# Kernel optimization log

Hardware: AMD Instinct MI355X
Metric: run time of the kernel (lower is better)

The kernel has to match this reference:

```python
import jax, jax.numpy as jnp
import numpy as np
from jax.scipy.special import logsumexp

S, L = 32768, 512  # seq_len, label_num


def setup_inputs() -> dict:
    key = jax.random.key(0)
    k1, k2, k3 = jax.random.split(key, 3)
    logit = jax.random.normal(k1, (S, L), dtype=jnp.float32)   # emissions [S, L]
    labels = jax.random.randint(k2, (S,), 0, L)                # gold path [S]
    T = jax.random.normal(k3, (L, L), dtype=jnp.float32)       # T[next, prev]
    return {"logit": logit, "labels": labels, "T": T}


def _crf_loss(logit, T, labels):
    # Forward algorithm: alpha_t[j] = logsumexp_i(alpha_{t-1}[i] + T[j, i]) + feat_t[j]
    alpha0 = logit[0]

    def step(alpha, feat):
        new_alpha = logsumexp(alpha[None, :] + T, axis=1) + feat  # [L]
        return new_alpha, None

    alpha_final, _ = jax.lax.scan(step, alpha0, logit[1:])
    log_Z = logsumexp(alpha_final)

    # Gold path score: feat_0[y0] + sum_{t>0} (feat_t[y_t] + T[y_t, y_{t-1}])
    emit = logit[0, labels[0]] + jnp.sum(logit[jnp.arange(1, logit.shape[0]), labels[1:]])
    trans = jnp.sum(T[labels[1:], labels[:-1]])
    gold = emit + trans
    return log_Z - gold


def reference(logit, labels, T):
    return _crf_loss(logit, T, labels)
```

## Files before the change

### kernel.cpp

```cpp
#include <hip/hip_runtime.h>
#include <stdint.h>


#define S_LEN 32768
#define L 512
#define CH 8
#define NCF 4096
#define NB  256
#define TPB 1024
#define LN448 6.104793232f
#define LN2   0.6931471806f

#define OFF_EAF  0
#define OFF_EAB  (256*1024)
#define OFF_G    (512*1024)
#define OFF_H    (OFF_G + NCF*512*2)
#define OFF_LSE  (OFF_H + NCF*512*2)
#define OFF_GOLD (OFF_LSE + (2*NCF+8)*4)

#define PL_A   0
#define PL_B   8192
#define SPA    16384
#define SPB    17664
#define LF     19456
#define SMEM_TOTAL (19456 + 4*32768)

typedef float v4f __attribute__((ext_vector_type(4)));

__device__ __forceinline__ float b2f(unsigned short u){
  return __uint_as_float(((unsigned)u) << 16);
}
__device__ __forceinline__ unsigned short f2b(float x){
  unsigned u = __float_as_uint(x);
  return (unsigned short)((u + 0x7fffu + ((u >> 16) & 1u)) >> 16);
}
__device__ __forceinline__ unsigned char to_fp8(float v){
  int u = __builtin_amdgcn_cvt_pk_fp8_f32(v, v, 0, false);
  return (unsigned char)(u & 0xff);
}

__device__ __forceinline__ void gl2lds16(const void* g, void* l){
  __builtin_amdgcn_global_load_lds(
      (const __attribute__((address_space(1))) void*)g,
      (__attribute__((address_space(3))) void*)l, 16, 0, 0);
}

__device__ __forceinline__ void lds_sync(){
  asm volatile("s_waitcnt lgkmcnt(0)" ::: "memory");
  __builtin_amdgcn_sched_barrier(0);
  __builtin_amdgcn_s_barrier();
  __builtin_amdgcn_sched_barrier(0);
}
__device__ __forceinline__ void sync2(){
  asm volatile("s_waitcnt vmcnt(2) lgkmcnt(0)" ::: "memory");
  __builtin_amdgcn_sched_barrier(0);
  __builtin_amdgcn_s_barrier();
  __builtin_amdgcn_sched_barrier(0);
}
__device__ __forceinline__ void sync0(){
  asm volatile("s_waitcnt vmcnt(0) lgkmcnt(0)" ::: "memory");
  __builtin_amdgcn_sched_barrier(0);
  __builtin_amdgcn_s_barrier();
  __builtin_amdgcn_sched_barrier(0);
}

__device__ __forceinline__ float waveMax(float v){
  #pragma unroll
  for (int off = 32; off >= 1; off >>= 1) v = fmaxf(v, __shfl_xor(v, off));
  return v;
}
__device__ __forceinline__ float waveSum(float v){
  #pragma unroll
  for (int off = 32; off >= 1; off >>= 1) v += __shfl_xor(v, off);
  return v;
}

__device__ __forceinline__ float blockSum16(float v, float* sred){
  #pragma unroll
  for (int off = 32; off >= 1; off >>= 1) v += __shfl_xor(v, off);
  int wid = threadIdx.x >> 6, lane = threadIdx.x & 63;
  if (lane == 0) sred[wid] = v;
  __syncthreads();
  if (threadIdx.x < 16) {
    float t = sred[threadIdx.x];
    t += __shfl_xor(t, 8); t += __shfl_xor(t, 4);
    t += __shfl_xor(t, 2); t += __shfl_xor(t, 1);
    if (threadIdx.x == 0) sred[16] = t;
  }
  __syncthreads();
  float r = sred[16];
  __syncthreads();
  return r;
}
__device__ __forceinline__ float blockSum8(float v, float* sred){
  #pragma unroll
  for (int off = 32; off >= 1; off >>= 1) v += __shfl_xor(v, off);
  int wid = threadIdx.x >> 6, lane = threadIdx.x & 63;
  if (lane == 0) sred[wid] = v;
  __syncthreads();
  if (threadIdx.x < 8) {
    float t = sred[threadIdx.x];
    t += __shfl_xor(t, 4); t += __shfl_xor(t, 2); t += __shfl_xor(t, 1);
    if (threadIdx.x == 0) sred[8] = t;
  }
  __syncthreads();
  float r = sred[8];
  __syncthreads();
  return r;
}

extern "C" __global__ __launch_bounds__(TPB)
void crf_prep(const float* __restrict__ logit,
              const int* __restrict__ labels,
              const float* __restrict__ T,
              unsigned char* __restrict__ EAf,
              unsigned char* __restrict__ EAb,
              float* __restrict__ part){
  __shared__ float sredG[17];
  const int tidx = threadIdx.x;
  {
    int tid = blockIdx.x*TPB + tidx;
    int r    = tid & 7;
    int lane = (tid >> 3) & 63;
    int kt   = (tid >> 9) & 15;
    int R16  = tid >> 13;
    int j = R16*16 + (lane & 15);
    int i = kt*32 + ((lane >> 4) << 3) + r;
    EAf[tid] = to_fp8(2.0f * __expf(T[j*L + i]));
    EAb[tid] = to_fp8(2.0f * __expf(T[i*L + j]));
  }
  {
    float acc = 0.f;
    if (tidx < 128) {
      int t = blockIdx.x*128 + tidx;
      int yt = labels[t];
      float v = logit[(size_t)t*L + yt];
      if (t > 0) v += T[yt*L + labels[t-1]];
      acc = v;
    }
    float s = blockSum16(acc, sredG);
    if (tidx == 0) part[blockIdx.x] = s;
  }
}

extern "C" __global__ __launch_bounds__(TPB, 4)
void crf_chunks(const float* __restrict__ logit,
                const unsigned char* __restrict__ EAf,
                const unsigned char* __restrict__ EAb,
                unsigned short* __restrict__ G,
                unsigned short* __restrict__ H){
  extern __shared__ __align__(16) char smem[];

  const int tidx = threadIdx.x;
  const int w    = tidx >> 6;
  const int lane = tidx & 63;
  const int quad = lane >> 4;
  const int cl   = lane & 15;
  const bool fwd = (blockIdx.x < NB/2);
  const int  b   = fwd ? blockIdx.x : (blockIdx.x - NB/2);
  const int  base = (fwd ? 0 : 1) + b*32;
  const int  cgA  = base + cl;
  const int  cgB  = cgA + 16;
  const int  cgcA = min(cgA, NCF-1);
  const int  cgcB = min(cgB, NCF-1);
  const bool isc0 = fwd && (cgA == 0);
  const int  jrow0 = w*32 + quad*4;

  const int  cgsA = min(base + w,      NCF-1);
  const int  cgsB = min(base + 16 + w, NCF-1);
  const unsigned so = ((unsigned)(lane*16)) ^ ((unsigned)((w & 7) << 4));

  const long* EAp = (const long*)(fwd ? EAf : EAb);
  long eA[2][16];
  #pragma unroll
  for (int mt = 0; mt < 2; ++mt)
    #pragma unroll
    for (int kt = 0; kt < 16; ++kt)
      eA[mt][kt] = EAp[(((w*2 + mt)*16) + kt)*64 + lane];

  const int pladdr = (jrow0 >> 5)*512 + ((((jrow0 >> 3) & 3)*16 + cl) << 3)
                   + (jrow0 & 7);
  const int bbb = lane*8;
  const int scl = (cl & 7) << 4;
  const int ib  = w*128 + quad*16;
  const int fa0 = LF + cl*2048 + (ib ^ scl);
  const int fa1 = LF + cl*2048 + ((ib + 64) ^ scl);

  auto stage = [&](int tile, int ks){
    int cgs = tile ? cgsB : cgsA;
    int t = fwd ? (cgs*CH + ks) : (cgs*CH + CH - 2 - ks);
    const char* row = (const char*)logit + (size_t)t*(L*4);
    char* dst = smem + (LF + ((ks & 1) << 16) + (tile << 15) + w*2048);
    gl2lds16(row + so, dst);
    gl2lds16(row + 1024 + so, dst + 1024);
  };
  auto wmax = [&](v4f x0, v4f x1, int spoff){
    float mx = fmaxf(fmaxf(fmaxf(x0[0],x0[1]),fmaxf(x0[2],x0[3])),
                     fmaxf(fmaxf(x1[0],x1[1]),fmaxf(x1[2],x1[3])));
    mx = fmaxf(mx, __shfl_xor(mx, 16));
    mx = fmaxf(mx, __shfl_xor(mx, 32));
    if (quad == 0) *(float*)(smem + spoff + cl*80 + w*4) = mx;
  };
  auto s2 = [&](v4f x0, v4f x1, int spoff, int ploff, float& m){
    const char* spb = smem + spoff + cl*80;
    float4 q0 = *(const float4*)spb;
    float4 q1 = *(const float4*)(spb + 16);
    float4 q2 = *(const float4*)(spb + 32);
    float4 q3 = *(const float4*)(spb + 48);
    float M = fmaxf(fmaxf(fmaxf(fmaxf(q0.x,q0.y),fmaxf(q0.z,q0.w)),
                          fmaxf(fmaxf(q1.x,q1.y),fmaxf(q1.z,q1.w))),
                    fmaxf(fmaxf(fmaxf(q2.x,q2.y),fmaxf(q2.z,q2.w)),
                          fmaxf(fmaxf(q3.x,q3.y),fmaxf(q3.z,q3.w))));
    float sc = 448.0f / M;
    int u0 = __builtin_amdgcn_cvt_pk_fp8_f32(x0[0]*sc, x0[1]*sc, 0, false);
    u0     = __builtin_amdgcn_cvt_pk_fp8_f32(x0[2]*sc, x0[3]*sc, u0, true);
    *(int*)(smem + ploff + pladdr) = u0;
    int u1 = __builtin_amdgcn_cvt_pk_fp8_f32(x1[0]*sc, x1[1]*sc, 0, false);
    u1     = __builtin_amdgcn_cvt_pk_fp8_f32(x1[2]*sc, x1[3]*sc, u1, true);
    *(int*)(smem + ploff + pladdr + 256) = u1;
    m += __logf(M) - LN448;
  };
  auto fmul = [&](v4f& x0, v4f& x1, int fbase, bool anchor){
    const char* fb = smem + fbase;
    float4 q0 = *(const float4*)(fb + fa0);
    float4 q1 = *(const float4*)(fb + fa1);
    float f0=__expf(q0.x), f1=__expf(q0.y), f2=__expf(q0.z), f3=__expf(q0.w);
    float g0=__expf(q1.x), g1=__expf(q1.y), g2=__expf(q1.z), g3=__expf(q1.w);
    if (anchor) {
      x0 = (v4f){f0,f1,f2,f3};  x1 = (v4f){g0,g1,g2,g3};
    } else {
      x0 = (v4f){x0[0]*f0, x0[1]*f1, x0[2]*f2, x0[3]*f3};
      x1 = (v4f){x1[0]*g0, x1[1]*g1, x1[2]*g2, x1[3]*g3};
    }
  };
  auto store_out = [&](v4f x0, v4f x1, float m, int cg, bool anchor){
    if (cg <= NCF-1) {
      float madj = m - (anchor ? (float)(CH-1) : (float)CH)*LN2;
      unsigned short* dst = (fwd ? G : H) + (size_t)cg*L + jrow0;
      unsigned long long pv =
           (unsigned long long)f2b(__logf(x0[0]) + madj)
        | ((unsigned long long)f2b(__logf(x0[1]) + madj) << 16)
        | ((unsigned long long)f2b(__logf(x0[2]) + madj) << 32)
        | ((unsigned long long)f2b(__logf(x0[3]) + madj) << 48);
      *(unsigned long long*)dst = pv;
      pv = (unsigned long long)f2b(__logf(x1[0]) + madj)
        | ((unsigned long long)f2b(__logf(x1[1]) + madj) << 16)
        | ((unsigned long long)f2b(__logf(x1[2]) + madj) << 32)
        | ((unsigned long long)f2b(__logf(x1[3]) + madj) << 48);
      *(unsigned long long*)(dst + 16) = pv;
    }
  };

  stage(0, 0);  stage(1, 0);

  v4f vA0, vA1, vB0, vB1;
  if (fwd) {
    vA0 = (v4f){1.f,1.f,1.f,1.f}; vA1 = vA0; vB0 = vA0; vB1 = vA0;
  } else {
    const float* ip = logit + (size_t)(cgcA*CH + CH - 1)*L + jrow0;
    float4 x0 = *(const float4*)ip, x1 = *(const float4*)(ip + 16);
    vA0 = (v4f){__expf(x0.x),__expf(x0.y),__expf(x0.z),__expf(x0.w)};
    vA1 = (v4f){__expf(x1.x),__expf(x1.y),__expf(x1.z),__expf(x1.w)};
    ip = logit + (size_t)(cgcB*CH + CH - 1)*L + jrow0;
    x0 = *(const float4*)ip; x1 = *(const float4*)(ip + 16);
    vB0 = (v4f){__expf(x0.x),__expf(x0.y),__expf(x0.z),__expf(x0.w)};
    vB1 = (v4f){__expf(x1.x),__expf(x1.y),__expf(x1.z),__expf(x1.w)};
  }
  float mA = 0.0f, mB = 0.0f;

  wmax(vA0, vA1, SPA);
  wmax(vB0, vB1, SPB);
  lds_sync();
  s2(vA0, vA1, SPA, PL_A, mA);
  sync2();

  #pragma unroll
  for (int k = 0; k < CH; ++k) {
    const bool last = (k == CH-1);
    {
      if (fwd ? (k+1 <= CH-1) : (k+1 <= CH-2)) stage(0, k+1);
      v4f a0 = (v4f){0.f,0.f,0.f,0.f};
      v4f a1 = (v4f){0.f,0.f,0.f,0.f};
      #pragma unroll
      for (int kt = 0; kt < 16; ++kt) {
        long bbv = *(const long*)(smem + PL_A + bbb + kt*512);
        a0 = __builtin_amdgcn_mfma_f32_16x16x32_fp8_fp8(eA[0][kt], bbv, a0, 0, 0, 0);
        a1 = __builtin_amdgcn_mfma_f32_16x16x32_fp8_fp8(eA[1][kt], bbv, a1, 0, 0, 0);
      }
      s2(vB0, vB1, SPB, PL_B, mB);
      if (fwd || !last) fmul(a0, a1, ((k & 1) << 16), k == 0 && isc0);
      if (k == 0 && isc0) mA = 0.0f;
      if (last) {
        store_out(a0, a1, mA, cgA, isc0);
      } else {
        vA0 = a0; vA1 = a1;
        wmax(vA0, vA1, SPA);
      }
      if (k >= CH-2) sync0(); else sync2();
    }
    {
      if (fwd ? (k+1 <= CH-1) : (k+1 <= CH-2)) stage(1, k+1);
      v4f b0 = (v4f){0.f,0.f,0.f,0.f};
      v4f b1 = (v4f){0.f,0.f,0.f,0.f};
      #pragma unroll
      for (int kt = 0; kt < 16; ++kt) {
        long bbv = *(const long*)(smem + PL_B + bbb + kt*512);
        b0 = __builtin_amdgcn_mfma_f32_16x16x32_fp8_fp8(eA[0][kt], bbv, b0, 0, 0, 0);
        b1 = __builtin_amdgcn_mfma_f32_16x16x32_fp8_fp8(eA[1][kt], bbv, b1, 0, 0, 0);
      }
      if (!last) s2(vA0, vA1, SPA, PL_A, mA);
      if (fwd || !last) fmul(b0, b1, ((k & 1) << 16) + 32768, false);
      if (last) {
        store_out(b0, b1, mB, cgB, false);
      } else {
        vB0 = b0; vB1 = b1;
        wmax(vB0, vB1, SPB);
        sync2();
      }
    }
  }
}

extern "C" __global__ __launch_bounds__(512)
void crf_lse(const unsigned short* __restrict__ G,
             const unsigned short* __restrict__ H,
             float* __restrict__ lsebuf){
  const int tidx = threadIdx.x;
  const int w    = tidx >> 6;
  const int lane = tidx & 63;
  const int g    = blockIdx.x*8 + w;
  const int j8   = lane*8;
  if (g == 0) {
    const unsigned short* p = G + (size_t)(NCF-1)*L + j8;
    ushort4 a = *(const ushort4*)p, bq = *(const ushort4*)(p + 4);
    float v[8] = { b2f(a.x),b2f(a.y),b2f(a.z),b2f(a.w),
                   b2f(bq.x),b2f(bq.y),b2f(bq.z),b2f(bq.w) };
    float mx = v[0];
    #pragma unroll
    for (int r = 1; r < 8; ++r) mx = fmaxf(mx, v[r]);
    mx = waveMax(mx);
    float s = 0.f;
    #pragma unroll
    for (int r = 0; r < 8; ++r) s += __expf(v[r] - mx);
    s = waveSum(s);
    if (lane == 0) lsebuf[2*NCF] = mx + __logf(s);
  } else {
    const unsigned short* hp = H + (size_t)g*L + j8;
    const unsigned short* gp = G + (size_t)(g-1)*L + j8;
    ushort4 ha = *(const ushort4*)hp, hb = *(const ushort4*)(hp + 4);
    ushort4 ga = *(const ushort4*)gp, gb = *(const ushort4*)(gp + 4);
    float hv[8] = { b2f(ha.x),b2f(ha.y),b2f(ha.z),b2f(ha.w),
                    b2f(hb.x),b2f(hb.y),b2f(hb.z),b2f(hb.w) };
    float gv[8] = { b2f(ga.x),b2f(ga.y),b2f(ga.z),b2f(ga.w),
                    b2f(gb.x),b2f(gb.y),b2f(gb.z),b2f(gb.w) };
    float m1 = -3.0e38f, m2 = -3.0e38f;
    #pragma unroll
    for (int r = 0; r < 8; ++r) {
      float a = hv[r] + gv[r];
      m1 = fmaxf(m1, a); m2 = fmaxf(m2, hv[r]);
    }
    m1 = waveMax(m1); m2 = waveMax(m2);
    float s1 = 0.f, s2 = 0.f;
    #pragma unroll
    for (int r = 0; r < 8; ++r) {
      s1 += __expf(hv[r] + gv[r] - m1);
      s2 += __expf(hv[r] - m2);
    }
    s1 = waveSum(s1); s2 = waveSum(s2);
    if (lane == 0) {
      lsebuf[g]       = m1 + __logf(s1);
      lsebuf[NCF + g] = m2 + __logf(s2);
    }
  }
}

extern "C" __global__ __launch_bounds__(512)
void crf_final(const float* __restrict__ lsebuf,
               const float* __restrict__ part,
               float* __restrict__ out){
  __shared__ float sredG[9];
  const int tidx = threadIdx.x;
  float acc = 0.f;
  for (int c = tidx; c < NCF; c += 512)
    if (c >= 1) acc += lsebuf[c] - lsebuf[NCF + c];
  if (tidx < NB) acc -= part[tidx];
  float s = blockSum8(acc, sredG);
  if (tidx == 0) out[0] = lsebuf[2*NCF] + s;
}

extern "C" void kernel_launch(void* const* d_in, const int* in_sizes, int n_in,
                              void* d_out, int out_size, void* d_ws, size_t ws_size,
                              hipStream_t stream){
  const float* logit = (const float*)d_in[0];
  const int* labels  = (const int*)d_in[1];
  const float* T     = (const float*)d_in[2];
  float* out = (float*)d_out;
  char* ws = (char*)d_ws;
  unsigned char* EAf = (unsigned char*)(ws + OFF_EAF);
  unsigned char* EAb = (unsigned char*)(ws + OFF_EAB);
  unsigned short* G  = (unsigned short*)(ws + OFF_G);
  unsigned short* H  = (unsigned short*)(ws + OFF_H);
  float* lsebuf = (float*)(ws + OFF_LSE);
  float* part   = (float*)(ws + OFF_GOLD);

  static bool attr_set = false;
  if (!attr_set) {
    (void)hipFuncSetAttribute((const void*)crf_chunks,
                        hipFuncAttributeMaxDynamicSharedMemorySize, SMEM_TOTAL);
    attr_set = true;
  }

  crf_prep  <<<NB, TPB, 0, stream>>>(logit, labels, T, EAf, EAb, part);
  crf_chunks<<<NB, TPB, SMEM_TOTAL, stream>>>(logit, EAf, EAb, G, H);
  crf_lse   <<<NCF/8, 512, 0, stream>>>(G, H, lsebuf);
  crf_final <<<1, 512, 0, stream>>>(lsebuf, part, out);
}
```

Before: 136.9 us.

## Merge ping-pong chain halves into one joint MFMA step per iteration

Replaces the staggered A/B ping-pong schedule, where one chain's MFMAs overlapped the other chain's reduction and normalisation, with a single step per iteration that runs both chains' MFMAs interleaved. Both chains then do their max-reduction and scaling together, so each iteration has two barriers instead of the earlier staggered sync2/sync0 pattern. The loop is no longer force-unrolled and every wait now drains all outstanding global loads (vmcnt(0)). This gives the scheduler more independent MFMA chains to interleave, but it removes the overlap between matrix work and the reduction phases and waits fully on staged loads each step.

```diff
diff --git a/kernel.cpp b/kernel.cpp
--- a/kernel.cpp
+++ b/kernel.cpp
@@ -47,12 +47,6 @@
 
 __device__ __forceinline__ void lds_sync(){
   asm volatile("s_waitcnt lgkmcnt(0)" ::: "memory");
-  __builtin_amdgcn_sched_barrier(0);
-  __builtin_amdgcn_s_barrier();
-  __builtin_amdgcn_sched_barrier(0);
-}
-__device__ __forceinline__ void sync2(){
-  asm volatile("s_waitcnt vmcnt(2) lgkmcnt(0)" ::: "memory");
   __builtin_amdgcn_sched_barrier(0);
   __builtin_amdgcn_s_barrier();
   __builtin_amdgcn_sched_barrier(0);
@@ -272,51 +266,44 @@
   wmax(vB0, vB1, SPB);
   lds_sync();
   s2(vA0, vA1, SPA, PL_A, mA);
-  sync2();
-
-  #pragma unroll
+  s2(vB0, vB1, SPB, PL_B, mB);
+  sync0();
+
   for (int k = 0; k < CH; ++k) {
     const bool last = (k == CH-1);
-    {
-      if (fwd ? (k+1 <= CH-1) : (k+1 <= CH-2)) stage(0, k+1);
-      v4f a0 = (v4f){0.f,0.f,0.f,0.f};
-      v4f a1 = (v4f){0.f,0.f,0.f,0.f};
-      #pragma unroll
-      for (int kt = 0; kt < 16; ++kt) {
-        long bbv = *(const long*)(smem + PL_A + bbb + kt*512);
-        a0 = __builtin_amdgcn_mfma_f32_16x16x32_fp8_fp8(eA[0][kt], bbv, a0, 0, 0, 0);
-        a1 = __builtin_amdgcn_mfma_f32_16x16x32_fp8_fp8(eA[1][kt], bbv, a1, 0, 0, 0);
-      }
+    const bool useF = fwd || !last;
+
+    if (fwd ? (k+1 <= CH-1) : (k+1 <= CH-2)) { stage(0, k+1); stage(1, k+1); }
+
+    v4f a0 = (v4f){0.f,0.f,0.f,0.f}, a1 = a0, b0 = a0, b1 = a0;
+    #pragma unroll
+    for (int kt = 0; kt < 16; ++kt) {
+      long bbA = *(const long*)(smem + PL_A + bbb + kt*512);
+      long bbB = *(const long*)(smem + PL_B + bbb + kt*512);
+      a0 = __builtin_amdgcn_mfma_f32_16x16x32_fp8_fp8(eA[0][kt], bbA, a0, 0, 0, 0);
+      a1 = __builtin_amdgcn_mfma_f32_16x16x32_fp8_fp8(eA[1][kt], bbA, a1, 0, 0, 0);
+      b0 = __builtin_amdgcn_mfma_f32_16x16x32_fp8_fp8(eA[0][kt], bbB, b0, 0, 0, 0);
+      b1 = __builtin_amdgcn_mfma_f32_16x16x32_fp8_fp8(eA[1][kt], bbB, b1, 0, 0, 0);
+    }
+
+    if (useF) {
+      const int fbase = (k & 1) << 16;
+      fmul(a0, a1, fbase, k == 0 && isc0);
+      fmul(b0, b1, fbase + 32768, false);
+      if (k == 0 && isc0) mA = 0.0f;
+    }
+
+    if (last) {
+      store_out(a0, a1, mA, cgA, isc0);
+      store_out(b0, b1, mB, cgB, false);
+    } else {
+      vA0 = a0; vA1 = a1; vB0 = b0; vB1 = b1;
+      wmax(vA0, vA1, SPA);
+      wmax(vB0, vB1, SPB);
+      lds_sync();
+      s2(vA0, vA1, SPA, PL_A, mA);
       s2(vB0, vB1, SPB, PL_B, mB);
-      if (fwd || !last) fmul(a0, a1, ((k & 1) << 16), k == 0 && isc0);
-      if (k == 0 && isc0) mA = 0.0f;
-      if (last) {
-        store_out(a0, a1, mA, cgA, isc0);
-      } else {
-        vA0 = a0; vA1 = a1;
-        wmax(vA0, vA1, SPA);
-      }
-      if (k >= CH-2) sync0(); else sync2();
-    }
-    {
-      if (fwd ? (k+1 <= CH-1) : (k+1 <= CH-2)) stage(1, k+1);
-      v4f b0 = (v4f){0.f,0.f,0.f,0.f};
-      v4f b1 = (v4f){0.f,0.f,0.f,0.f};
-      #pragma unroll
-      for (int kt = 0; kt < 16; ++kt) {
-        long bbv = *(const long*)(smem + PL_B + bbb + kt*512);
-        b0 = __builtin_amdgcn_mfma_f32_16x16x32_fp8_fp8(eA[0][kt], bbv, b0, 0, 0, 0);
-        b1 = __builtin_amdgcn_mfma_f32_16x16x32_fp8_fp8(eA[1][kt], bbv, b1, 0, 0, 0);
-      }
-      if (!last) s2(vA0, vA1, SPA, PL_A, mA);
-      if (fwd || !last) fmul(b0, b1, ((k & 1) << 16) + 32768, false);
-      if (last) {
-        store_out(b0, b1, mB, cgB, false);
-      } else {
-        vB0 = b0; vB1 = b1;
-        wmax(vB0, vB1, SPB);
-        sync2();
-      }
+      sync0();
     }
   }
 }
```

Result: slower. 141.0 us (+3.0%).
